# Optimization experiments

Measured on AMD Instinct MI355X. Metric: run time of the kernel, lower is better.

Reference implementation:

```python
import jax, jax.numpy as jnp
import numpy as np

N, D, NUM_CLASSES = 8192, 64, 16
EPS = 1e-7


def setup_inputs() -> dict:
    key = jax.random.key(0)
    k1, k2 = jax.random.split(key)
    raw = jax.random.normal(k1, (N, D), dtype=jnp.float32)
    # project into the open Poincare ball: norm < 0.9
    nrm = jnp.linalg.norm(raw, axis=-1, keepdims=True)
    points = raw * (0.9 / (1.0 + nrm))
    labels = jax.random.randint(k2, (N,), 0, NUM_CLASSES, dtype=jnp.int64)
    return {"points": points, "labels": labels}


def _poincare_dist_matrix(x):
    # d(x,y) = arccosh(1 + 2||x-y||^2 / ((1-||x||^2)(1-||y||^2)))
    sq = jnp.sum(x * x, axis=-1)                      # [N]
    sqdist = jnp.maximum(sq[:, None] + sq[None, :] - 2.0 * (x @ x.T), 0.0)  # [N,N]
    denom = jnp.maximum((1.0 - sq)[:, None] * (1.0 - sq)[None, :], EPS)
    arg = jnp.maximum(1.0 + 2.0 * sqdist / denom, 1.0 + EPS)
    return jnp.arccosh(arg)


def reference(points, labels):
    d = _poincare_dist_matrix(points)                 # [N,N]
    logits = -d
    n = logits.shape[0]
    diag = jnp.eye(n, dtype=bool)
    neg_inf = jnp.finfo(logits.dtype).min
    # log A_i = logsumexp_{a != i} (-d_ia)
    logA = jax.nn.logsumexp(jnp.where(diag, neg_inf, logits), axis=1)  # [N]
    pos = (labels[:, None] == labels[None, :]) & (~diag)               # [N,N]
    P = jnp.sum(pos, axis=1).astype(logits.dtype)                      # [N]
    p_sum = jnp.sum(jnp.where(pos, logits - logA[:, None], 0.0), axis=1)
    return jnp.sum(-p_sum / P)
```

## Files before the change

### kernel.cpp

```cpp
#include <hip/hip_runtime.h>

#define NPTS 8192
#define DIM 64
#define EPSF 1e-7f
#define LN2F 0.69314718055994531f
#define NBLK 1056

typedef unsigned short u16;
typedef __attribute__((ext_vector_type(8))) short bf16x8;
typedef __attribute__((ext_vector_type(8))) unsigned short u16x8;
typedef __attribute__((ext_vector_type(4))) float f32x4;
typedef __attribute__((ext_vector_type(2))) float f32x2;

__global__ void prep_kernel(const float* __restrict__ x, const int* __restrict__ labels,
                            u16* __restrict__ hi,
                            float4* __restrict__ meta,
                            float* __restrict__ S, float* __restrict__ T,
                            float* __restrict__ out) {
    int g = blockIdx.x * blockDim.x + threadIdx.x;
    int row = g >> 3, sub = g & 7;
    const float* xp = x + row * DIM + sub * 8;
    float v[8];
    float s = 0.f;
#pragma unroll
    for (int k = 0; k < 8; k++) { v[k] = xp[k]; s = fmaf(v[k], v[k], s); }
    s += __shfl_xor(s, 1);
    s += __shfl_xor(s, 2);
    s += __shfl_xor(s, 4);
    u16x8 h;
#pragma unroll
    for (int k = 0; k < 8; k++) {
        unsigned int bits = __float_as_uint(v[k]);
        unsigned int r = bits + 0x7FFFu + ((bits >> 16) & 1u);
        h[k] = (u16)(r >> 16);
    }
    *(u16x8*)(hi + row * DIM + sub * 8) = h;
    if (sub == 0) {
        float r = 1.0f / (1.0f - s);
        meta[row] = make_float4(-0.5f * s, r, -4.0f * r, (float)labels[row]);
    } else if (sub == 1) {
        S[row] = 0.f;
    } else if (sub == 2) {
        T[row] = 0.f;
    }
    if (g == 3) out[0] = 0.f;
}

__device__ __forceinline__ int cumtiles(int b) { return 65 * b - b * b; }

__global__ void __launch_bounds__(256, 4) pair_mfma(
        const u16* __restrict__ hi,
        const float4* __restrict__ meta,
        float* __restrict__ Sarr, float* __restrict__ Tarr) {
    __shared__ float slabS[4][128], slabT[4][128];

    int tid = threadIdx.x;
    int wave = tid >> 6, lane = tid & 63;
    int quad = lane >> 4, l15 = lane & 15;

    int bid2 = blockIdx.x;
    int bid = bid2 >> 1;
    int half = bid2 & 1;
    int by = (int)((65.0f - __builtin_amdgcn_sqrtf(4225.0f - 4.0f * (float)bid)) * 0.5f);
    while (cumtiles(by + 1) <= bid) by++;
    while (cumtiles(by) > bid) by--;
    int off = bid - cumtiles(by);
    int bx = 2 * by + off;
    bool full = (off >= 2);

    int i0 = bx * 128 + wave * 32;
    int j0 = by * 256;
    int jbase = j0 + half * 128;

    bf16x8 a_hi[2][2];
#pragma unroll
    for (int it = 0; it < 2; it++)
#pragma unroll
        for (int ks = 0; ks < 2; ks++) {
            int aoff = (i0 + it * 16 + l15) * DIM + ks * 32 + quad * 8;
            a_hi[it][ks] = *(const bf16x8*)(hi + aoff);
        }

    f32x4 hsqi4[2];
    f32x2 rcp2[4];
    float labi[8];
#pragma unroll
    for (int it = 0; it < 2; it++)
#pragma unroll
        for (int r = 0; r < 4; r++) {
            float4 m = meta[i0 + it * 16 + quad * 4 + r];
            hsqi4[it][r] = m.x;
            rcp2[it * 2 + (r >> 1)][r & 1] = m.y;
            labi[it * 4 + r] = m.w;
        }

    if (full) {
        slabS[wave][lane] = 0.f;       slabT[wave][lane] = 0.f;
        slabS[wave][lane + 64] = 0.f;  slabT[wave][lane + 64] = 0.f;
    }

    f32x2 Sx2[4], Tx2[4];
#pragma unroll
    for (int k = 0; k < 4; k++) { Sx2[k] = (f32x2){0.f, 0.f}; Tx2[k] = (f32x2){0.f, 0.f}; }

    bf16x8 bh[2][2];
    float4 mjb[2];
    {
        int boff = (jbase + l15) * DIM + quad * 8;
        bh[0][0] = *(const bf16x8*)(hi + boff);
        bh[0][1] = *(const bf16x8*)(hi + boff + 32);
        mjb[0] = meta[jbase + l15];
    }

#pragma unroll 2
    for (int t = 0; t < 8; t++) {
        int cur = t & 1, nxt = cur ^ 1;
        if (t < 7) {
            int jgn = jbase + (t + 1) * 16 + l15;
            int boff = jgn * DIM + quad * 8;
            bh[nxt][0] = *(const bf16x8*)(hi + boff);
            bh[nxt][1] = *(const bf16x8*)(hi + boff + 32);
            mjb[nxt] = meta[jgn];
        }
        float4 mj = mjb[cur];

        f32x2 sSum = (f32x2){0.f, 0.f}, tSum = (f32x2){0.f, 0.f};
#pragma unroll
        for (int it = 0; it < 2; it++) {
            f32x4 acc = hsqi4[it] + mj.x;
            acc = __builtin_amdgcn_mfma_f32_16x16x32_bf16(a_hi[it][0], bh[cur][0], acc, 0, 0, 0);
            acc = __builtin_amdgcn_mfma_f32_16x16x32_bf16(a_hi[it][1], bh[cur][1], acc, 0, 0, 0);

#pragma unroll
            for (int g = 0; g < 2; g++) {
                f32x2 D = (f32x2){acc[2 * g], acc[2 * g + 1]};
                f32x2 u = (D * rcp2[it * 2 + g]) * mj.z;
                u = __builtin_elementwise_max(u, (f32x2){EPSF, EPSF});
                f32x2 arg = u * u + (u + u);
                f32x2 srt = (f32x2){__builtin_amdgcn_sqrtf(arg.x), __builtin_amdgcn_sqrtf(arg.y)};
                f32x2 opu = u + 1.0f;
                f32x2 st = opu - srt;
                f32x2 w1 = opu + srt;
                f32x2 l2;
                l2.x = __builtin_amdgcn_logf(w1.x);
                l2.y = __builtin_amdgcn_logf(w1.y);
                f32x2 tv;
                tv.x = (mj.w == labi[it * 4 + 2 * g]) ? l2.x : 0.0f;
                tv.y = (mj.w == labi[it * 4 + 2 * g + 1]) ? l2.y : 0.0f;
                Sx2[it * 2 + g] += st;
                Tx2[it * 2 + g] += tv;
                sSum += st;
                tSum += tv;
            }
        }

        if (full) {
            float pS = sSum.x + sSum.y, pT = tSum.x + tSum.y;
            pS += __shfl_xor(pS, 16); pS += __shfl_xor(pS, 32);
            pT += __shfl_xor(pT, 16); pT += __shfl_xor(pT, 32);
            if (quad == 0) {
                int c = t * 16 + l15;
                slabS[wave][c] += pS;
                slabT[wave][c] += pT;
            }
        }
    }

    float Sx[8], Tx[8];
#pragma unroll
    for (int k = 0; k < 4; k++) {
        Sx[2 * k] = Sx2[k].x; Sx[2 * k + 1] = Sx2[k].y;
        Tx[2 * k] = Tx2[k].x; Tx[2 * k + 1] = Tx2[k].y;
    }
#pragma unroll
    for (int r = 0; r < 8; r++) {
#pragma unroll
        for (int m = 1; m < 16; m <<= 1) {
            Sx[r] += __shfl_xor(Sx[r], m);
            Tx[r] += __shfl_xor(Tx[r], m);
        }
    }
    if (l15 == 0) {
#pragma unroll
        for (int it = 0; it < 2; it++)
#pragma unroll
            for (int r = 0; r < 4; r++) {
                int row = i0 + it * 16 + quad * 4 + r;
                atomicAdd(&Sarr[row], Sx[it * 4 + r]);
                atomicAdd(&Tarr[row], Tx[it * 4 + r]);
            }
    }

    if (full) {
        __syncthreads();
        if (tid < 128) {
            float s = slabS[0][tid] + slabS[1][tid] + slabS[2][tid] + slabS[3][tid];
            float tt = slabT[0][tid] + slabT[1][tid] + slabT[2][tid] + slabT[3][tid];
            atomicAdd(&Sarr[jbase + tid], s);
            atomicAdd(&Tarr[jbase + tid], tt);
        }
    }
}

__global__ void __launch_bounds__(256) finalize_kernel(
        const float* __restrict__ S, const float* __restrict__ T,
        const int* __restrict__ labels, float* __restrict__ out) {
    __shared__ int hist[16][16];
    __shared__ float cntf[16];
    __shared__ float red[256];
    int tid = threadIdx.x;
    hist[tid >> 4][tid & 15] = 0;
    __syncthreads();
    int rep = tid & 15;
    for (int i = tid; i < NPTS; i += 256)
        atomicAdd(&hist[rep][labels[i]], 1);
    __syncthreads();
    if (tid < 16) {
        int s = 0;
#pragma unroll
        for (int k = 0; k < 16; k++) s += hist[k][tid];
        cntf[tid] = (float)(s - 1);
    }
    __syncthreads();

    float s0 = __builtin_amdgcn_sqrtf(EPSF * (2.0f + EPSF));
    float st0 = 1.0f + EPSF - s0;
    float l20 = __builtin_amdgcn_logf(1.0f + EPSF + s0);
    int i = blockIdx.x * 256 + tid;
    float loss = __logf(S[i] - st0) + (T[i] - l20) * LN2F / cntf[labels[i]];
    red[tid] = loss;
    __syncthreads();
    for (int s = 128; s > 0; s >>= 1) {
        if (tid < s) red[tid] += red[tid + s];
        __syncthreads();
    }
    if (tid == 0) atomicAdd(out, red[0]);
}

extern "C" void kernel_launch(void* const* d_in, const int* in_sizes, int n_in,
                              void* d_out, int out_size, void* d_ws, size_t ws_size,
                              hipStream_t stream) {
    const float* x = (const float*)d_in[0];
    const int* labels = (const int*)d_in[1];

    u16* hi = (u16*)d_ws;
    float4* meta = (float4*)(hi + NPTS * DIM);
    float* S = (float*)(meta + NPTS);
    float* T = S + NPTS;

    prep_kernel<<<(NPTS * 8) / 256, 256, 0, stream>>>(x, labels, hi, meta, S, T, (float*)d_out);

    pair_mfma<<<2 * NBLK, 256, 0, stream>>>(hi, meta, S, T);

    finalize_kernel<<<NPTS / 256, 256, 0, stream>>>(S, T, labels, (float*)d_out);
}
```

Measured before the change: 102.7 us.

## Replace global atomic row accumulation with per-block partial buffers reduced in finalize

The pair kernel no longer issues atomicAdds into the per-row S/T arrays. Each block now writes its row and column partial sums to its own slot in workspace buffers, and the finalize kernel gathers those partials per row by walking the triangular tile schedule. This removes atomic contention and the zero-initialisation in prep. In exchange the finalize kernel does more strided global reads, and the workspace footprint grows.

```diff
diff --git a/kernel.cpp b/kernel.cpp
--- a/kernel.cpp
+++ b/kernel.cpp
@@ -15,7 +15,6 @@
 __global__ void prep_kernel(const float* __restrict__ x, const int* __restrict__ labels,
                             u16* __restrict__ hi,
                             float4* __restrict__ meta,
-                            float* __restrict__ S, float* __restrict__ T,
                             float* __restrict__ out) {
     int g = blockIdx.x * blockDim.x + threadIdx.x;
     int row = g >> 3, sub = g & 7;
@@ -38,10 +37,6 @@
     if (sub == 0) {
         float r = 1.0f / (1.0f - s);
         meta[row] = make_float4(-0.5f * s, r, -4.0f * r, (float)labels[row]);
-    } else if (sub == 1) {
-        S[row] = 0.f;
-    } else if (sub == 2) {
-        T[row] = 0.f;
     }
     if (g == 3) out[0] = 0.f;
 }
@@ -51,7 +46,7 @@
 __global__ void __launch_bounds__(256, 4) pair_mfma(
         const u16* __restrict__ hi,
         const float4* __restrict__ meta,
-        float* __restrict__ Sarr, float* __restrict__ Tarr) {
+        float* __restrict__ Pi, float* __restrict__ Pj) {
     __shared__ float slabS[4][128], slabT[4][128];
 
     int tid = threadIdx.x;
@@ -180,34 +175,36 @@
             Tx[r] += __shfl_xor(Tx[r], m);
         }
     }
+    float* PiB = Pi + (size_t)bid2 * 256;
     if (l15 == 0) {
 #pragma unroll
         for (int it = 0; it < 2; it++)
 #pragma unroll
             for (int r = 0; r < 4; r++) {
-                int row = i0 + it * 16 + quad * 4 + r;
-                atomicAdd(&Sarr[row], Sx[it * 4 + r]);
-                atomicAdd(&Tarr[row], Tx[it * 4 + r]);
+                int rowb = wave * 32 + it * 16 + quad * 4 + r;
+                PiB[rowb] = Sx[it * 4 + r];
+                PiB[128 + rowb] = Tx[it * 4 + r];
             }
     }
 
     if (full) {
         __syncthreads();
+        float* PjB = Pj + (size_t)bid2 * 256;
         if (tid < 128) {
-            float s = slabS[0][tid] + slabS[1][tid] + slabS[2][tid] + slabS[3][tid];
-            float tt = slabT[0][tid] + slabT[1][tid] + slabT[2][tid] + slabT[3][tid];
-            atomicAdd(&Sarr[jbase + tid], s);
-            atomicAdd(&Tarr[jbase + tid], tt);
+            PjB[tid] = slabS[0][tid] + slabS[1][tid] + slabS[2][tid] + slabS[3][tid];
+        } else {
+            int c = tid - 128;
+            PjB[tid] = slabT[0][c] + slabT[1][c] + slabT[2][c] + slabT[3][c];
         }
     }
 }
 
 __global__ void __launch_bounds__(256) finalize_kernel(
-        const float* __restrict__ S, const float* __restrict__ T,
+        const float* __restrict__ Pi, const float* __restrict__ Pj,
         const int* __restrict__ labels, float* __restrict__ out) {
     __shared__ int hist[16][16];
     __shared__ float cntf[16];
-    __shared__ float red[256];
+    __shared__ float redS[4][64], redT[4][64];
     int tid = threadIdx.x;
     hist[tid >> 4][tid & 15] = 0;
     __syncthreads();
@@ -221,20 +218,39 @@
         for (int k = 0; k < 16; k++) s += hist[k][tid];
         cntf[tid] = (float)(s - 1);
     }
+
+    int slice = tid >> 6, pl = tid & 63;
+    int i = blockIdx.x * 64 + pl;
+    int bx = i >> 7, r = i & 127;
+    float s = 0.f, t = 0.f;
+    for (int by = slice; by <= (bx >> 1); by += 4) {
+        int c2 = (cumtiles(by) + (bx - 2 * by)) * 512;
+        s += Pi[c2 + r] + Pi[c2 + 256 + r];
+        t += Pi[c2 + 128 + r] + Pi[c2 + 384 + r];
+    }
+    int byj = bx >> 1, half = bx & 1;
+    int jmax = 64 - 2 * byj;
+    int cbase = cumtiles(byj);
+    for (int off = 2 + slice; off < jmax; off += 4) {
+        int c2 = ((cbase + off) * 2 + half) * 256;
+        s += Pj[c2 + r];
+        t += Pj[c2 + 128 + r];
+    }
+    redS[slice][pl] = s;
+    redT[slice][pl] = t;
     __syncthreads();
-
-    float s0 = __builtin_amdgcn_sqrtf(EPSF * (2.0f + EPSF));
-    float st0 = 1.0f + EPSF - s0;
-    float l20 = __builtin_amdgcn_logf(1.0f + EPSF + s0);
-    int i = blockIdx.x * 256 + tid;
-    float loss = __logf(S[i] - st0) + (T[i] - l20) * LN2F / cntf[labels[i]];
-    red[tid] = loss;
-    __syncthreads();
-    for (int s = 128; s > 0; s >>= 1) {
-        if (tid < s) red[tid] += red[tid + s];
-        __syncthreads();
-    }
-    if (tid == 0) atomicAdd(out, red[0]);
+    if (tid < 64) {
+        float S = redS[0][tid] + redS[1][tid] + redS[2][tid] + redS[3][tid];
+        float T = redT[0][tid] + redT[1][tid] + redT[2][tid] + redT[3][tid];
+        float s0 = __builtin_amdgcn_sqrtf(EPSF * (2.0f + EPSF));
+        float st0 = 1.0f + EPSF - s0;
+        float l20 = __builtin_amdgcn_logf(1.0f + EPSF + s0);
+        int ii = blockIdx.x * 64 + tid;
+        float loss = __logf(S - st0) + (T - l20) * LN2F / cntf[labels[ii]];
+#pragma unroll
+        for (int m = 1; m < 64; m <<= 1) loss += __shfl_xor(loss, m);
+        if (tid == 0) atomicAdd(out, loss);
+    }
 }
 
 extern "C" void kernel_launch(void* const* d_in, const int* in_sizes, int n_in,
@@ -245,12 +261,12 @@
 
     u16* hi = (u16*)d_ws;
     float4* meta = (float4*)(hi + NPTS * DIM);
-    float* S = (float*)(meta + NPTS);
-    float* T = S + NPTS;
-
-    prep_kernel<<<(NPTS * 8) / 256, 256, 0, stream>>>(x, labels, hi, meta, S, T, (float*)d_out);
-
-    pair_mfma<<<2 * NBLK, 256, 0, stream>>>(hi, meta, S, T);
-
-    finalize_kernel<<<NPTS / 256, 256, 0, stream>>>(S, T, labels, (float*)d_out);
-}
+    float* Pi = (float*)(meta + NPTS);
+    float* Pj = Pi + 2 * NBLK * 256;
+
+    prep_kernel<<<(NPTS * 8) / 256, 256, 0, stream>>>(x, labels, hi, meta, (float*)d_out);
+
+    pair_mfma<<<2 * NBLK, 256, 0, stream>>>(hi, meta, Pi, Pj);
+
+    finalize_kernel<<<NPTS / 64, 256, 0, stream>>>(Pi, Pj, labels, (float*)d_out);
+}
```

New measurement: 104.6 us. No clear change (+1.8%).
